# Kernel optimization log

Measured on AMD Instinct MI355X. Metric: run time of the kernel, lower is better.

Reference implementation:

```python
import jax, jax.numpy as jnp
import numpy as np

BETA = 1.0
DECAY = 0.95


def setup_inputs() -> dict:
    key = jax.random.key(0)
    ks = jax.random.split(key, 10)
    B, S, D = 8, 2048, 1024
    M, d = 4096, 256
    sc_in = 1.0 / np.sqrt(D)
    sc_slot = 1.0 / np.sqrt(d)
    return {
        "x": jax.random.normal(ks[0], (B, S, D), jnp.float32),
        "memory": jax.random.normal(ks[1], (B, M, d), jnp.float32) * 0.01,
        "Wq": jax.random.normal(ks[2], (D, d), jnp.float32) * sc_in,
        "bq": jnp.zeros((d,), jnp.float32),
        "Wv": jax.random.normal(ks[3], (D, d), jnp.float32) * sc_in,
        "bv": jnp.zeros((d,), jnp.float32),
        "Wo": jax.random.normal(ks[4], (d, D), jnp.float32) * sc_slot,
        "bo": jnp.zeros((D,), jnp.float32),
        "Wg": jax.random.normal(ks[5], (D, 1), jnp.float32) * sc_in,
        "bg": jnp.zeros((1,), jnp.float32),
    }


def reference(x, memory, Wq, bq, Wv, bv, Wo, bo, Wg, bg):
    # ---- shared summary + query ----
    x_summary = jnp.mean(x, axis=1)                      # [B, D]
    query = x_summary @ Wq + bq                          # [B, d]

    # ---- read: Hopfield retrieval against memory[0] (shared patterns) ----
    patterns = memory[0]                                 # [M, d]
    read_scores = BETA * (query @ patterns.T)            # [B, M]
    read_attn = jax.nn.softmax(read_scores, axis=-1)
    retrieved = read_attn @ patterns                     # [B, d]
    read_out = retrieved @ Wo + bo                       # [B, D]
    x_augmented = x + read_out[:, None, :]               # broadcast over seq

    # ---- write: gated EMA update to per-batch memory ----
    write_value = x_summary @ Wv + bv                    # [B, d]
    write_gate = jax.nn.sigmoid(x_summary @ Wg + bg)     # [B, 1]
    w_scores = BETA * jnp.einsum('bd,bmd->bm', query, memory)
    w_attn = jax.nn.softmax(w_scores, axis=-1)           # [B, M]
    update = write_gate[:, :, None] * write_value[:, None, :]   # [B, 1, d]
    weighted_update = w_attn[:, :, None] * update        # [B, M, d]
    memory_new = DECAY * memory + (1.0 - DECAY) * weighted_update

    return x_augmented, memory_new
```

## Files before the change

### kernel.cpp

```cpp
#include <hip/hip_runtime.h>
#include <math.h>

#define BB 8
#define SS 2048
#define DD 1024
#define MM 4096
#define dd 256
#define NCH 64
#define CS (SS/NCH)
#define KSL 32

#define OFF_PART  0
#define OFF_PP    524288
#define OFF_PG    655360
#define OFF_Q     655616
#define OFF_WV    657664
#define OFF_GATE  659712
#define OFF_COMBO 659720
#define OFF_SUMS  659728
#define OFF_SC    659744
#define OFF_PRET  725280
#define OFF_RET   856352
#define OFF_ROUT  858400

__global__ void k1(const float* __restrict__ x, float* __restrict__ ws) {
    int blk = blockIdx.x;
    int chunk = blk & 63;
    int b = blk >> 6;
    int t = threadIdx.x;
    const float4* x4 = (const float4*)(x + ((size_t)b*SS + (size_t)chunk*CS)*DD);
    float4 a = make_float4(0.f,0.f,0.f,0.f);
    #pragma unroll 8
    for (int s = 0; s < CS; ++s) {
        float4 v = x4[s*(DD/4) + t];
        a.x += v.x; a.y += v.y; a.z += v.z; a.w += v.w;
    }
    ((float4*)(ws + OFF_PART))[(size_t)(b*NCH + chunk)*256 + t] = a;
}

__global__ void k2(const float* __restrict__ Wq, const float* __restrict__ Wv,
                   const float* __restrict__ Wg, float* __restrict__ ws) {
    __shared__ float xs[BB][KSL];
    int blk = blockIdx.x;
    int ks = blk & 31;
    int which = blk >> 5;
    int t = threadIdx.x;
    int e = t >> 2;
    int b = e >> 3;
    int kk = e & 7;
    int k4 = ks*8 + kk;
    int q = t & 3;
    const float4* p4 = (const float4*)(ws + OFF_PART);
    float4 a = make_float4(0.f,0.f,0.f,0.f);
    #pragma unroll
    for (int i = 0; i < 16; ++i) {
        float4 v = p4[(size_t)(b*NCH + q*16 + i)*256 + k4];
        a.x += v.x; a.y += v.y; a.z += v.z; a.w += v.w;
    }
    #pragma unroll
    for (int off = 1; off < 4; off <<= 1) {
        a.x += __shfl_xor(a.x, off); a.y += __shfl_xor(a.y, off);
        a.z += __shfl_xor(a.z, off); a.w += __shfl_xor(a.w, off);
    }
    if (q == 0) {
        xs[b][kk*4+0] = a.x * (1.0f/SS); xs[b][kk*4+1] = a.y * (1.0f/SS);
        xs[b][kk*4+2] = a.z * (1.0f/SS); xs[b][kk*4+3] = a.w * (1.0f/SS);
    }
    __syncthreads();
    const float* W = which ? Wv : Wq;
    float acc[BB];
    #pragma unroll
    for (int b2 = 0; b2 < BB; ++b2) acc[b2] = 0.f;
    #pragma unroll 4
    for (int kk2 = 0; kk2 < KSL; ++kk2) {
        float w = W[(size_t)(ks*KSL + kk2)*dd + t];
        #pragma unroll
        for (int b2 = 0; b2 < BB; ++b2) acc[b2] += xs[b2][kk2] * w;
    }
    #pragma unroll
    for (int b2 = 0; b2 < BB; ++b2)
        ws[OFF_PP + (size_t)(which*KSL + ks)*2048 + b2*dd + t] = acc[b2];
    if (which == 0) {
        int gb = t >> 5, gk = t & 31;
        float v = xs[gb][gk] * Wg[ks*KSL + gk];
        #pragma unroll
        for (int off = 16; off > 0; off >>= 1) v += __shfl_xor(v, off);
        if (gk == 0) ws[OFF_PG + gb*32 + ks] = v;
    }
}

__global__ void k3(const float* __restrict__ bq, const float* __restrict__ bv,
                   const float* __restrict__ bg, float* __restrict__ ws) {
    int blk = blockIdx.x;
    int t = threadIdx.x;
    if (blk < 16) {
        int which = blk >> 3, b = blk & 7;
        float acc = 0.f;
        #pragma unroll
        for (int ks = 0; ks < KSL; ++ks)
            acc += ws[OFF_PP + (size_t)(which*KSL + ks)*2048 + b*dd + t];
        acc += which ? bv[t] : bq[t];
        ws[(which ? OFF_WV : OFF_Q) + b*dd + t] = acc;
    } else if (t < BB) {
        float g = 0.f;
        #pragma unroll
        for (int i = 0; i < 32; ++i) g += ws[OFF_PG + t*32 + i];
        ws[OFF_GATE + t] = 1.f / (1.f + __expf(-(g + bg[0])));
    }
}

__global__ void k4(const float* __restrict__ memory, float* __restrict__ ws) {
    int wave = threadIdx.x >> 6;
    int lane = threadIdx.x & 63;
    int task = blockIdx.x*4 + wave;
    int m = task & (MM-1);
    int b = (task >> 12) & 7;
    int which = task >> 15;
    const float* row = (which == 0) ? (memory + (size_t)m*dd)
                                    : (memory + ((size_t)b*MM + m)*dd);
    const float4 a  = ((const float4*)row)[lane];
    const float4 qv = ((const float4*)(ws + OFF_Q + b*dd))[lane];
    float p = a.x*qv.x + a.y*qv.y + a.z*qv.z + a.w*qv.w;
    #pragma unroll
    for (int off = 32; off > 0; off >>= 1) p += __shfl_xor(p, off);
    if (lane == 0) ws[OFF_SC + (size_t)(which*BB + b)*MM + m] = __expf(p);
}

__global__ void k5(const float* __restrict__ memory, float* __restrict__ ws) {
    __shared__ float red[256];
    int blk = blockIdx.x;
    int t = threadIdx.x;
    if (blk < 16) {
        const float4* p = (const float4*)(ws + OFF_SC + (size_t)blk*MM);
        float s = 0.f;
        #pragma unroll
        for (int i = 0; i < 4; ++i) {
            float4 v = p[i*256 + t];
            s += v.x + v.y + v.z + v.w;
        }
        red[t] = s; __syncthreads();
        for (int s2 = 128; s2 > 0; s2 >>= 1) {
            if (t < s2) red[t] += red[t + s2];
            __syncthreads();
        }
        if (t == 0) ws[OFF_SUMS + blk] = red[0];
    } else {
        int idx = blk - 16;
        int mc = idx & 63;
        int b = idx >> 6;
        if (t < 64) red[t] = ws[OFF_SC + (size_t)b*MM + mc*64 + t];
        __syncthreads();
        float acc = 0.f;
        const float* pat = memory + (size_t)mc*64*dd + t;
        #pragma unroll 8
        for (int i = 0; i < 64; ++i) acc += red[i] * pat[(size_t)i*dd];
        ws[OFF_PRET + (size_t)(b*64 + mc)*dd + t] = acc;
    }
}

__global__ void k6(float* __restrict__ ws) {
    int b = blockIdx.x;
    int t = threadIdx.x;
    float acc = 0.f;
    #pragma unroll 8
    for (int mc = 0; mc < 64; ++mc)
        acc += ws[OFF_PRET + (size_t)(b*64 + mc)*dd + t];
    ws[OFF_RET + b*dd + t] = acc / ws[OFF_SUMS + b];
    if (t == 0)
        ws[OFF_COMBO + b] = 0.05f * ws[OFF_GATE + b] / ws[OFF_SUMS + BB + b];
}

__global__ void k7(const float* __restrict__ Wo, const float* __restrict__ bo,
                   float* __restrict__ ws) {
    __shared__ float ret[dd];
    __shared__ float red[256];
    int blk = blockIdx.x;
    int cb = blk & 15;
    int b = blk >> 4;
    int t = threadIdx.x;
    ret[t] = ws[OFF_RET + b*dd + t];
    __syncthreads();
    int c = t & 63, jr = t >> 6;
    float acc = 0.f;
    #pragma unroll 8
    for (int jj = 0; jj < 64; ++jj) {
        int j = jr*64 + jj;
        acc += ret[j] * Wo[(size_t)j*DD + cb*64 + c];
    }
    red[t] = acc; __syncthreads();
    if (t < 64) {
        float o = red[t] + red[t+64] + red[t+128] + red[t+192] + bo[cb*64 + t];
        ws[OFF_ROUT + (size_t)b*DD + cb*64 + t] = o;
    }
}

__global__ void k8(const float* __restrict__ x, const float* __restrict__ memory,
                   const float* __restrict__ ws, float* __restrict__ out) {
    const int NA = BB*SS*DD/4;
    const int NT = NA + BB*MM*dd/4;
    const float4* x4 = (const float4*)x;
    const float4* m4 = (const float4*)memory;
    const float4* r4 = (const float4*)(ws + OFF_ROUT);
    const float4* w4 = (const float4*)(ws + OFF_WV);
    float4* o4 = (float4*)out;
    int stride = gridDim.x * blockDim.x;
    for (int i = blockIdx.x*blockDim.x + threadIdx.x; i < NT; i += stride) {
        if (i < NA) {
            int b = i >> 19;
            int c = i & 255;
            float4 xv = x4[i];
            float4 rv = r4[(b << 8) + c];
            o4[i] = make_float4(xv.x+rv.x, xv.y+rv.y, xv.z+rv.z, xv.w+rv.w);
        } else {
            int j = i - NA;
            int b = j >> 18;
            int m = (j >> 6) & (MM-1);
            int d4 = j & 63;
            float coeff = ws[OFF_COMBO + b] * ws[OFF_SC + (size_t)(BB + b)*MM + m];
            float4 wv = w4[(b << 6) + d4];
            float4 mv = m4[j];
            o4[i] = make_float4(0.95f*mv.x + coeff*wv.x,
                                0.95f*mv.y + coeff*wv.y,
                                0.95f*mv.z + coeff*wv.z,
                                0.95f*mv.w + coeff*wv.w);
        }
    }
}

extern "C" void kernel_launch(void* const* d_in, const int* in_sizes, int n_in,
                              void* d_out, int out_size, void* d_ws, size_t ws_size,
                              hipStream_t stream) {
    const float* x      = (const float*)d_in[0];
    const float* memory = (const float*)d_in[1];
    const float* Wq     = (const float*)d_in[2];
    const float* bq     = (const float*)d_in[3];
    const float* Wv     = (const float*)d_in[4];
    const float* bv     = (const float*)d_in[5];
    const float* Wo     = (const float*)d_in[6];
    const float* bo     = (const float*)d_in[7];
    const float* Wg     = (const float*)d_in[8];
    const float* bg     = (const float*)d_in[9];
    float* out = (float*)d_out;
    float* ws  = (float*)d_ws;

    k1<<<BB*NCH, 256, 0, stream>>>(x, ws);
    k2<<<2*KSL, 256, 0, stream>>>(Wq, Wv, Wg, ws);
    k3<<<17, 256, 0, stream>>>(bq, bv, bg, ws);
    k4<<<2*BB*MM/4, 256, 0, stream>>>(memory, ws);
    k5<<<16 + BB*64, 256, 0, stream>>>(memory, ws);
    k6<<<BB, 256, 0, stream>>>(ws);
    k7<<<BB*16, 256, 0, stream>>>(Wo, bo, ws);
    k8<<<4096, 256, 0, stream>>>(x, memory, ws, out);
}
```

Measured before the change: 78.36 us.

## Fuse projection split-K and reduction kernels, fold retrieval normalization into Wo matvec

Merges the split-K projection kernel and its reduction kernel into a single kernel. Each of 16 blocks now reduces the chunk partials for one batch and computes the full 1024-long dot product for Wq or Wv, and 8 extra blocks compute the gate. The retrieval sum and normalization kernel is removed by having each Wo block redo that reduction itself. This drops two kernel launches and their global round trips. The cost is much less parallelism in the projection (24 blocks, each streaming a full 1 MB weight matrix serially) and the retrieval reduction being repeated 16 times per batch.

```diff
diff --git a/kernel.cpp b/kernel.cpp
--- a/kernel.cpp
+++ b/kernel.cpp
@@ -8,20 +8,16 @@
 #define dd 256
 #define NCH 64
 #define CS (SS/NCH)
-#define KSL 32
 
 #define OFF_PART  0
-#define OFF_PP    524288
-#define OFF_PG    655360
-#define OFF_Q     655616
-#define OFF_WV    657664
-#define OFF_GATE  659712
-#define OFF_COMBO 659720
-#define OFF_SUMS  659728
-#define OFF_SC    659744
-#define OFF_PRET  725280
-#define OFF_RET   856352
-#define OFF_ROUT  858400
+#define OFF_Q     524288
+#define OFF_WV    526336
+#define OFF_GATE  528384
+#define OFF_COMBO 528392
+#define OFF_SUMS  528400
+#define OFF_SC    528416
+#define OFF_PRET  593952
+#define OFF_ROUT  725024
 
 __global__ void k1(const float* __restrict__ x, float* __restrict__ ws) {
     int blk = blockIdx.x;
@@ -38,74 +34,53 @@
     ((float4*)(ws + OFF_PART))[(size_t)(b*NCH + chunk)*256 + t] = a;
 }
 
-__global__ void k2(const float* __restrict__ Wq, const float* __restrict__ Wv,
-                   const float* __restrict__ Wg, float* __restrict__ ws) {
-    __shared__ float xs[BB][KSL];
-    int blk = blockIdx.x;
-    int ks = blk & 31;
-    int which = blk >> 5;
-    int t = threadIdx.x;
-    int e = t >> 2;
-    int b = e >> 3;
-    int kk = e & 7;
-    int k4 = ks*8 + kk;
-    int q = t & 3;
+__global__ void k2(const float* __restrict__ Wq, const float* __restrict__ bq,
+                   const float* __restrict__ Wv, const float* __restrict__ bv,
+                   const float* __restrict__ Wg, const float* __restrict__ bg,
+                   float* __restrict__ ws) {
+    int blk = blockIdx.x;
+    int t = threadIdx.x;
     const float4* p4 = (const float4*)(ws + OFF_PART);
-    float4 a = make_float4(0.f,0.f,0.f,0.f);
-    #pragma unroll
-    for (int i = 0; i < 16; ++i) {
-        float4 v = p4[(size_t)(b*NCH + q*16 + i)*256 + k4];
-        a.x += v.x; a.y += v.y; a.z += v.z; a.w += v.w;
-    }
-    #pragma unroll
-    for (int off = 1; off < 4; off <<= 1) {
-        a.x += __shfl_xor(a.x, off); a.y += __shfl_xor(a.y, off);
-        a.z += __shfl_xor(a.z, off); a.w += __shfl_xor(a.w, off);
-    }
-    if (q == 0) {
-        xs[b][kk*4+0] = a.x * (1.0f/SS); xs[b][kk*4+1] = a.y * (1.0f/SS);
-        xs[b][kk*4+2] = a.z * (1.0f/SS); xs[b][kk*4+3] = a.w * (1.0f/SS);
-    }
-    __syncthreads();
-    const float* W = which ? Wv : Wq;
-    float acc[BB];
-    #pragma unroll
-    for (int b2 = 0; b2 < BB; ++b2) acc[b2] = 0.f;
-    #pragma unroll 4
-    for (int kk2 = 0; kk2 < KSL; ++kk2) {
-        float w = W[(size_t)(ks*KSL + kk2)*dd + t];
-        #pragma unroll
-        for (int b2 = 0; b2 < BB; ++b2) acc[b2] += xs[b2][kk2] * w;
-    }
-    #pragma unroll
-    for (int b2 = 0; b2 < BB; ++b2)
-        ws[OFF_PP + (size_t)(which*KSL + ks)*2048 + b2*dd + t] = acc[b2];
-    if (which == 0) {
-        int gb = t >> 5, gk = t & 31;
-        float v = xs[gb][gk] * Wg[ks*KSL + gk];
-        #pragma unroll
-        for (int off = 16; off > 0; off >>= 1) v += __shfl_xor(v, off);
-        if (gk == 0) ws[OFF_PG + gb*32 + ks] = v;
-    }
-}
-
-__global__ void k3(const float* __restrict__ bq, const float* __restrict__ bv,
-                   const float* __restrict__ bg, float* __restrict__ ws) {
-    int blk = blockIdx.x;
-    int t = threadIdx.x;
     if (blk < 16) {
-        int which = blk >> 3, b = blk & 7;
+        __shared__ float4 xs4[256];
+        int which = blk & 1;
+        int b = blk >> 1;
+        float4 a = make_float4(0.f,0.f,0.f,0.f);
+        #pragma unroll 8
+        for (int c = 0; c < NCH; ++c) {
+            float4 v = p4[(size_t)(b*NCH + c)*256 + t];
+            a.x += v.x; a.y += v.y; a.z += v.z; a.w += v.w;
+        }
+        xs4[t] = make_float4(a.x*(1.f/SS), a.y*(1.f/SS), a.z*(1.f/SS), a.w*(1.f/SS));
+        __syncthreads();
+        const float* xs = (const float*)xs4;
+        const float* W = which ? Wv : Wq;
+        float a0=0.f, a1=0.f, a2=0.f, a3=0.f;
+        for (int k = 0; k < DD; k += 4) {
+            a0 += xs[k]   * W[(size_t)k*dd + t];
+            a1 += xs[k+1] * W[(size_t)(k+1)*dd + t];
+            a2 += xs[k+2] * W[(size_t)(k+2)*dd + t];
+            a3 += xs[k+3] * W[(size_t)(k+3)*dd + t];
+        }
+        float acc = (a0+a1) + (a2+a3) + (which ? bv[t] : bq[t]);
+        ws[(which ? OFF_WV : OFF_Q) + b*dd + t] = acc;
+    } else {
+        __shared__ float red[256];
+        int b = blk - 16;
+        float4 wg = ((const float4*)Wg)[t];
         float acc = 0.f;
-        #pragma unroll
-        for (int ks = 0; ks < KSL; ++ks)
-            acc += ws[OFF_PP + (size_t)(which*KSL + ks)*2048 + b*dd + t];
-        acc += which ? bv[t] : bq[t];
-        ws[(which ? OFF_WV : OFF_Q) + b*dd + t] = acc;
-    } else if (t < BB) {
-        float g = 0.f;
-        #pragma unroll
-        for (int i = 0; i < 32; ++i) g += ws[OFF_PG + t*32 + i];
-        ws[OFF_GATE + t] = 1.f / (1.f + __expf(-(g + bg[0])));
+        #pragma unroll 8
+        for (int c = 0; c < NCH; ++c) {
+            float4 v = p4[(size_t)(b*NCH + c)*256 + t];
+            acc += v.x*wg.x + v.y*wg.y + v.z*wg.z + v.w*wg.w;
+        }
+        red[t] = acc; __syncthreads();
+        for (int s2 = 128; s2 > 0; s2 >>= 1) {
+            if (t < s2) red[t] += red[t + s2];
+            __syncthreads();
+        }
+        if (t == 0)
+            ws[OFF_GATE + b] = 1.f / (1.f + __expf(-(red[0]*(1.f/SS) + bg[0])));
     }
 }
 
@@ -158,18 +133,6 @@
     }
 }
 
-__global__ void k6(float* __restrict__ ws) {
-    int b = blockIdx.x;
-    int t = threadIdx.x;
-    float acc = 0.f;
-    #pragma unroll 8
-    for (int mc = 0; mc < 64; ++mc)
-        acc += ws[OFF_PRET + (size_t)(b*64 + mc)*dd + t];
-    ws[OFF_RET + b*dd + t] = acc / ws[OFF_SUMS + b];
-    if (t == 0)
-        ws[OFF_COMBO + b] = 0.05f * ws[OFF_GATE + b] / ws[OFF_SUMS + BB + b];
-}
-
 __global__ void k7(const float* __restrict__ Wo, const float* __restrict__ bo,
                    float* __restrict__ ws) {
     __shared__ float ret[dd];
@@ -178,7 +141,13 @@
     int cb = blk & 15;
     int b = blk >> 4;
     int t = threadIdx.x;
-    ret[t] = ws[OFF_RET + b*dd + t];
+    float acc0 = 0.f;
+    #pragma unroll 8
+    for (int mc = 0; mc < 64; ++mc)
+        acc0 += ws[OFF_PRET + (size_t)(b*64 + mc)*dd + t];
+    ret[t] = acc0 / ws[OFF_SUMS + b];
+    if (cb == 0 && t == 0)
+        ws[OFF_COMBO + b] = 0.05f * ws[OFF_GATE + b] / ws[OFF_SUMS + BB + b];
     __syncthreads();
     int c = t & 63, jr = t >> 6;
     float acc = 0.f;
@@ -189,8 +158,8 @@
     }
     red[t] = acc; __syncthreads();
     if (t < 64) {
-        float o = red[t] + red[t+64] + red[t+128] + red[t+192] + bo[cb*64 + t];
-        ws[OFF_ROUT + (size_t)b*DD + cb*64 + t] = o;
+        ws[OFF_ROUT + (size_t)b*DD + cb*64 + t] =
+            red[t] + red[t+64] + red[t+128] + red[t+192] + bo[cb*64 + t];
     }
 }
 
@@ -244,11 +213,9 @@
     float* ws  = (float*)d_ws;
 
     k1<<<BB*NCH, 256, 0, stream>>>(x, ws);
-    k2<<<2*KSL, 256, 0, stream>>>(Wq, Wv, Wg, ws);
-    k3<<<17, 256, 0, stream>>>(bq, bv, bg, ws);
+    k2<<<24, 256, 0, stream>>>(Wq, bq, Wv, bv, Wg, bg, ws);
     k4<<<2*BB*MM/4, 256, 0, stream>>>(memory, ws);
     k5<<<16 + BB*64, 256, 0, stream>>>(memory, ws);
-    k6<<<BB, 256, 0, stream>>>(ws);
     k7<<<BB*16, 256, 0, stream>>>(Wo, bo, ws);
     k8<<<4096, 256, 0, stream>>>(x, memory, ws, out);
 }
```

Result: slower. 95.74 us (+22.2%).
